# Optimization experiments

Hardware: AMD Instinct MI355X
Metric: run time of the kernel (lower is better)

Reference implementation:

```python
import jax, jax.numpy as jnp
import numpy as np

B, D, H, N, M, S = 64, 256, 512, 16384, 64, 3
EPS = 1e-4


def setup_inputs() -> dict:
    key = jax.random.key(0)
    ks = jax.random.split(key, 20)
    rn = lambda k, shape, sc=1.0: jax.random.normal(k, shape, dtype=jnp.float32) * sc
    z = lambda n: jnp.zeros((n,), jnp.float32)
    sc = 0.05
    return {
        "inp": rn(ks[0], (B, D)),
        "h_tm1": rn(ks[1], (B, H), 0.1),
        "c_tm1": rn(ks[2], (B, H), 0.1),
        "read_tm1": jax.nn.softmax(rn(ks[3], (B, N)), axis=-1),
        "write_tm1": jax.nn.softmax(rn(ks[4], (B, N)), axis=-1),
        "memory": rn(ks[5], (B, N, M), 0.1),
        "W_ih": rn(ks[6], (4 * H, D + M), sc), "b_ih": z(4 * H),
        "W_hh": rn(ks[7], (4 * H, H), sc), "b_hh": z(4 * H),
        "W_rk": rn(ks[8], (M, H), sc), "b_rk": z(M),
        "W_wk": rn(ks[9], (M, H), sc), "b_wk": z(M),
        "W_rc": rn(ks[10], (3, H), sc), "b_rc": z(3),
        "W_wc": rn(ks[11], (3, H), sc), "b_wc": z(3),
        "W_rs": rn(ks[12], (S, H), sc), "b_rs": z(S),
        "W_ws": rn(ks[13], (S, H), sc), "b_ws": z(S),
        "W_w": rn(ks[14], (2 * M, H), sc), "b_w": z(2 * M),
    }


def _head_params(h, Wk, bk, Wc, bc, Ws, bs):
    k = jnp.tanh(h @ Wk.T + bk)                 # [B, M] key
    c = h @ Wc.T + bc                           # [B, 3] beta/g/gamma raw
    s = jax.nn.softmax(h @ Ws.T + bs, axis=-1)  # [B, S] shift dist
    beta = jax.nn.relu(c[:, 0:1]) + EPS
    g = jax.nn.sigmoid(c[:, 1:2])
    gamma = jax.nn.relu(c[:, 2:3]) + 1.0 + EPS
    return k, s, beta, g, gamma


def _address(memory, w_tm1, k, s, beta, g, gamma):
    # content addressing: beta-scaled cosine similarity, softmax over slots
    dot = jnp.einsum('bm,bnm->bn', k, memory)                    # [B, N]
    nM = jnp.sqrt(jnp.sum(memory * memory, axis=-1)) + EPS       # [B, N]
    nk = jnp.sqrt(jnp.sum(k * k, axis=-1, keepdims=True)) + EPS  # [B, 1]
    content = jax.nn.softmax(beta * dot / (nM * nk), axis=-1)
    # interpolation with previous head
    inter = g * content + (1.0 - g) * w_tm1                      # [B, N]
    # circular shift conv: out[j] = sum_r s[r] * inter[(j + r - (S-1)) mod N]
    shifted = jnp.stack([jnp.roll(inter, S - 1 - r, axis=1) for r in range(S)], axis=-1)  # [B, N, S]
    conv = jnp.einsum('bns,bs->bn', shifted, s)
    # sharpening
    sharp = jnp.maximum(conv, 1e-8) ** gamma
    return sharp / jnp.sum(sharp, axis=1, keepdims=True)


def reference(inp, h_tm1, c_tm1, read_tm1, write_tm1, memory,
              W_ih, b_ih, W_hh, b_hh, W_rk, b_rk, W_wk, b_wk,
              W_rc, b_rc, W_wc, b_wc, W_rs, b_rs, W_ws, b_ws, W_w, b_w):
    # read head addressed from previous hidden state
    rk, rs, rbeta, rg, rgamma = _head_params(h_tm1, W_rk, b_rk, W_rc, b_rc, W_rs, b_rs)
    read_head = _address(memory, read_tm1, rk, rs, rbeta, rg, rgamma)
    M_read = jnp.einsum('bn,bnm->bm', read_head, memory)         # [B, M]
    # LSTMCell controller (torch gate order i, f, g, o)
    x = jnp.concatenate([inp, M_read], axis=1)
    gates = x @ W_ih.T + b_ih + h_tm1 @ W_hh.T + b_hh
    i, f, gg, o = jnp.split(gates, 4, axis=1)
    c_t = jax.nn.sigmoid(f) * c_tm1 + jax.nn.sigmoid(i) * jnp.tanh(gg)
    h_t = jax.nn.sigmoid(o) * jnp.tanh(c_t)
    # write head addressed from new hidden state
    wk, ws, wbeta, wg, wgamma = _head_params(h_t, W_wk, b_wk, W_wc, b_wc, W_ws, b_ws)
    write_head = _address(memory, write_tm1, wk, ws, wbeta, wg, wgamma)
    wa = h_t @ W_w.T + b_w
    e = jax.nn.sigmoid(wa[:, :M])                                # erase [B, M]
    a = wa[:, M:]                                                # add   [B, M]
    ww = write_head[:, :, None]                                  # [B, N, 1]
    M_out = memory * (1.0 - ww * e[:, None, :]) + ww * a[:, None, :]
    return (h_t, c_t, read_head, write_head, M_out)
```

## Files before the change

### kernel.cpp

```cpp
#include <hip/hip_runtime.h>
#include <hip/hip_bf16.h>
#include <math.h>

#define B_  64
#define D_  256
#define H_  512
#define N_  16384
#define M_  64
#define S_  3
#define EPS_ 1e-4f

__device__ __forceinline__ float sigmoidf_(float x) { return 1.0f / (1.0f + expf(-x)); }

template <bool WITH_W>
__global__ __launch_bounds__(256) void head_params_kernel(
    const float* __restrict__ h,
    const float* __restrict__ Wk, const float* __restrict__ bk,
    const float* __restrict__ Wc, const float* __restrict__ bc,
    const float* __restrict__ Ws, const float* __restrict__ bs,
    const float* __restrict__ Ww, const float* __restrict__ bw,
    float* __restrict__ k_out, float* __restrict__ nk_out,
    float* __restrict__ s_out,
    float* __restrict__ beta_out, float* __restrict__ g_out, float* __restrict__ gamma_out,
    float* __restrict__ e_out, float* __restrict__ a_out)
{
    const int b = blockIdx.x;
    const int tid = threadIdx.x;
    const int lane = tid & 63;
    const int wid = tid >> 6;
    __shared__ float raw[198];

    float h8[8];
    #pragma unroll
    for (int j = 0; j < 8; ++j) h8[j] = h[b * H_ + lane + 64 * j];

    const int count = WITH_W ? 198 : 70;
    for (int r = wid; r < count; r += 4) {
        const float* wrow;
        float bias;
        if (r < 64)       { wrow = Wk + r * H_;        bias = bk[r]; }
        else if (r < 67)  { wrow = Wc + (r - 64) * H_; bias = bc[r - 64]; }
        else if (r < 70)  { wrow = Ws + (r - 67) * H_; bias = bs[r - 67]; }
        else              { wrow = Ww + (r - 70) * H_; bias = bw[r - 70]; }
        float acc = 0.f;
        #pragma unroll
        for (int j = 0; j < 8; ++j) acc += wrow[lane + 64 * j] * h8[j];
        for (int off = 32; off >= 1; off >>= 1) acc += __shfl_xor(acc, off);
        if (lane == 0) raw[r] = acc + bias;
    }
    __syncthreads();

    if (tid < 64) {
        float kv = tanhf(raw[tid]);
        k_out[b * 64 + tid] = kv;
        float sq = kv * kv;
        for (int off = 32; off >= 1; off >>= 1) sq += __shfl_xor(sq, off);
        if (tid == 0) nk_out[b] = sqrtf(sq) + EPS_;
    } else if (tid == 64) {
        float c0 = raw[64], c1 = raw[65], c2 = raw[66];
        beta_out[b]  = fmaxf(c0, 0.f) + EPS_;
        g_out[b]     = sigmoidf_(c1);
        gamma_out[b] = fmaxf(c2, 0.f) + 1.f + EPS_;
    } else if (tid == 65) {
        float s0 = raw[67], s1 = raw[68], s2 = raw[69];
        float mx = fmaxf(s0, fmaxf(s1, s2));
        float e0 = expf(s0 - mx), e1 = expf(s1 - mx), e2 = expf(s2 - mx);
        float inv = 1.f / (e0 + e1 + e2);
        s_out[b * 3 + 0] = e0 * inv;
        s_out[b * 3 + 1] = e1 * inv;
        s_out[b * 3 + 2] = e2 * inv;
    }
    if (WITH_W && tid >= 128 && tid < 192) {
        int m = tid - 128;
        e_out[b * 64 + m] = sigmoidf_(raw[70 + m]);
        a_out[b * 64 + m] = raw[134 + m];
    }
}

template <bool COMPUTE_NM>
__global__ __launch_bounds__(256) void dot_kernel(
    const float* __restrict__ memory,
    const float* __restrict__ k,
    float* __restrict__ dot,
    float* __restrict__ nM)
{
    const int tid = threadIdx.x;
    const int lane = tid & 63;
    const int wid = tid >> 6;
    const int grp = lane >> 4;
    const int m16 = lane & 15;
    const int b = blockIdx.x >> 8;
    const int nbase = (blockIdx.x & 255) * 64;
    const float4 k4 = ((const float4*)(k + b * 64))[m16];
    const int slot = wid * 4 + grp;
    const size_t bbase = (size_t)b * N_;
    #pragma unroll
    for (int it = 0; it < 4; ++it) {
        const int n = nbase + it * 16 + slot;
        const float4 m4 = ((const float4*)(memory + (bbase + n) * 64))[m16];
        float d  = m4.x * k4.x + m4.y * k4.y + m4.z * k4.z + m4.w * k4.w;
        float sq = m4.x * m4.x + m4.y * m4.y + m4.z * m4.z + m4.w * m4.w;
        for (int off = 8; off >= 1; off >>= 1) {
            d += __shfl_xor(d, off);
            if (COMPUTE_NM) sq += __shfl_xor(sq, off);
        }
        if (m16 == 0) {
            dot[bbase + n] = d;
            if (COMPUTE_NM) nM[bbase + n] = sqrtf(sq) + EPS_;
        }
    }
}

__global__ __launch_bounds__(1024) void address_kernel(
    const float* __restrict__ dot,
    const float* __restrict__ nM,
    const float* __restrict__ w_tm1,
    const float* __restrict__ nk_a,
    const float* __restrict__ beta_a, const float* __restrict__ g_a,
    const float* __restrict__ gamma_a, const float* __restrict__ s_a,
    float* __restrict__ head_out)
{
    __shared__ float lds[N_];
    const int tid = threadIdx.x;
    const int b = blockIdx.x;
    const size_t base = (size_t)b * N_;
    const float beta = beta_a[b], g = g_a[b], gamma = gamma_a[b], nk = nk_a[b];
    const float s0 = s_a[b * 3 + 0], s1 = s_a[b * 3 + 1], s2 = s_a[b * 3 + 2];

    float lg[16];
    float lmax = -1e30f;
    #pragma unroll
    for (int t = 0; t < 16; ++t) {
        const int n = t * 1024 + tid;
        const float x = beta * dot[base + n] / (nM[base + n] * nk);
        lg[t] = x;
        lmax = fmaxf(lmax, x);
    }
    for (int off = 32; off >= 1; off >>= 1) lmax = fmaxf(lmax, __shfl_xor(lmax, off));
    if ((tid & 63) == 0) lds[tid >> 6] = lmax;
    __syncthreads();
    if (tid == 0) {
        float v = lds[0];
        for (int i = 1; i < 16; ++i) v = fmaxf(v, lds[i]);
        lds[16] = v;
    }
    __syncthreads();
    const float gmax = lds[16];

    float lsum = 0.f;
    #pragma unroll
    for (int t = 0; t < 16; ++t) { lg[t] = expf(lg[t] - gmax); lsum += lg[t]; }
    for (int off = 32; off >= 1; off >>= 1) lsum += __shfl_xor(lsum, off);
    if ((tid & 63) == 0) lds[tid >> 6] = lsum;
    __syncthreads();
    if (tid == 0) {
        float v = 0.f;
        for (int i = 0; i < 16; ++i) v += lds[i];
        lds[16] = v;
    }
    __syncthreads();
    const float inv_sum = 1.f / lds[16];
    __syncthreads();

    #pragma unroll
    for (int t = 0; t < 16; ++t) {
        const int n = t * 1024 + tid;
        lds[n] = g * lg[t] * inv_sum + (1.f - g) * w_tm1[base + n];
    }
    __syncthreads();

    float sh[16];
    float lsum2 = 0.f;
    #pragma unroll
    for (int t = 0; t < 16; ++t) {
        const int n = t * 1024 + tid;
        const float conv = s2 * lds[n] + s1 * lds[(n + N_ - 1) & (N_ - 1)]
                         + s0 * lds[(n + N_ - 2) & (N_ - 1)];
        const float v = powf(fmaxf(conv, 1e-8f), gamma);
        sh[t] = v;
        lsum2 += v;
    }
    __syncthreads();
    for (int off = 32; off >= 1; off >>= 1) lsum2 += __shfl_xor(lsum2, off);
    if ((tid & 63) == 0) lds[tid >> 6] = lsum2;
    __syncthreads();
    if (tid == 0) {
        float v = 0.f;
        for (int i = 0; i < 16; ++i) v += lds[i];
        lds[16] = v;
    }
    __syncthreads();
    const float inv2 = 1.f / lds[16];
    #pragma unroll
    for (int t = 0; t < 16; ++t) head_out[base + t * 1024 + tid] = sh[t] * inv2;
}

__global__ __launch_bounds__(256) void m_read_kernel(
    const float* __restrict__ memory,
    const float* __restrict__ head,
    float* __restrict__ M_read)
{
    const int tid = threadIdx.x;
    const int lane = tid & 63;
    const int wid = tid >> 6;
    const int grp = lane >> 4;
    const int m16 = lane & 15;
    const int b = blockIdx.x >> 6;
    const int nbase = (blockIdx.x & 63) * 256;
    const int slot = wid * 4 + grp;
    const size_t bbase = (size_t)b * N_;
    float4 acc = make_float4(0.f, 0.f, 0.f, 0.f);
    #pragma unroll 4
    for (int it = 0; it < 16; ++it) {
        const int n = nbase + it * 16 + slot;
        const float w = head[bbase + n];
        const float4 m4 = ((const float4*)(memory + (bbase + n) * 64))[m16];
        acc.x += w * m4.x; acc.y += w * m4.y; acc.z += w * m4.z; acc.w += w * m4.w;
    }
    for (int off = 32; off >= 16; off >>= 1) {
        acc.x += __shfl_xor(acc.x, off);
        acc.y += __shfl_xor(acc.y, off);
        acc.z += __shfl_xor(acc.z, off);
        acc.w += __shfl_xor(acc.w, off);
    }
    __shared__ float4 part[64];
    if (lane < 16) part[wid * 16 + lane] = acc;
    __syncthreads();
    if (tid < 16) {
        float4 t = part[tid];
        for (int w = 1; w < 4; ++w) {
            const float4 p = part[w * 16 + tid];
            t.x += p.x; t.y += p.y; t.z += p.z; t.w += p.w;
        }
        atomicAdd(&M_read[b * 64 + tid * 4 + 0], t.x);
        atomicAdd(&M_read[b * 64 + tid * 4 + 1], t.y);
        atomicAdd(&M_read[b * 64 + tid * 4 + 2], t.z);
        atomicAdd(&M_read[b * 64 + tid * 4 + 3], t.w);
    }
}

__global__ __launch_bounds__(256) void gates_splitk_kernel(
    const float* __restrict__ inp,
    const float* __restrict__ M_read,
    const float* __restrict__ h_tm1,
    const float* __restrict__ W_ih,
    const float* __restrict__ W_hh,
    float* __restrict__ gates)
{
    __shared__ __align__(16) float Xsm[64][68];
    __shared__ __align__(16) float Wsm[64][68];
    const int tid = threadIdx.x;
    const int jb = blockIdx.x & 31;
    const int c  = blockIdx.x >> 5;
    const int j0 = jb * 64;

    #pragma unroll
    for (int i = 0; i < 4; ++i) {
        const int e = i * 256 + tid;
        const int row = e >> 4;
        const int c4 = e & 15;
        const float* xrow;
        if (c < 4)       xrow = inp    + row * 256 + c * 64;
        else if (c == 4) xrow = M_read + row * 64;
        else             xrow = h_tm1  + row * 512 + (c - 5) * 64;
        const float4 v = ((const float4*)xrow)[c4];
        const int kl = c4 * 4;
        Xsm[kl + 0][row] = v.x; Xsm[kl + 1][row] = v.y;
        Xsm[kl + 2][row] = v.z; Xsm[kl + 3][row] = v.w;
    }
    #pragma unroll
    for (int i = 0; i < 4; ++i) {
        const int e = i * 256 + tid;
        const int row = e >> 4;
        const int c4 = e & 15;
        const float* wrow;
        if (c < 5) wrow = W_ih + (j0 + row) * 320 + c * 64;
        else       wrow = W_hh + (j0 + row) * 512 + (c - 5) * 64;
        const float4 v = ((const float4*)wrow)[c4];
        const int kl = c4 * 4;
        Wsm[kl + 0][row] = v.x; Wsm[kl + 1][row] = v.y;
        Wsm[kl + 2][row] = v.z; Wsm[kl + 3][row] = v.w;
    }
    __syncthreads();

    const int tx = tid & 15, ty = tid >> 4;
    float acc[4][4] = {};
    #pragma unroll
    for (int k = 0; k < 64; ++k) {
        const float4 av = *((const float4*)&Xsm[k][ty * 4]);
        const float4 wv = *((const float4*)&Wsm[k][tx * 4]);
        acc[0][0] += av.x * wv.x; acc[0][1] += av.x * wv.y; acc[0][2] += av.x * wv.z; acc[0][3] += av.x * wv.w;
        acc[1][0] += av.y * wv.x; acc[1][1] += av.y * wv.y; acc[1][2] += av.y * wv.z; acc[1][3] += av.y * wv.w;
        acc[2][0] += av.z * wv.x; acc[2][1] += av.z * wv.y; acc[2][2] += av.z * wv.z; acc[2][3] += av.z * wv.w;
        acc[3][0] += av.w * wv.x; acc[3][1] += av.w * wv.y; acc[3][2] += av.w * wv.z; acc[3][3] += av.w * wv.w;
    }
    #pragma unroll
    for (int bi = 0; bi < 4; ++bi) {
        const int b = ty * 4 + bi;
        #pragma unroll
        for (int ji = 0; ji < 4; ++ji) {
            atomicAdd(&gates[b * 2048 + j0 + tx * 4 + ji], acc[bi][ji]);
        }
    }
}

__global__ __launch_bounds__(256) void lstm_kernel(
    const float* __restrict__ gates,
    const float* __restrict__ b_ih, const float* __restrict__ b_hh,
    const float* __restrict__ c_tm1,
    float* __restrict__ h_out, float* __restrict__ c_out)
{
    const int idx = blockIdx.x * 256 + threadIdx.x;
    const int b = idx >> 9, j = idx & 511;
    const float* gr = gates + b * 2048;
    const float i_ = sigmoidf_(gr[j]        + b_ih[j]        + b_hh[j]);
    const float f_ = sigmoidf_(gr[512 + j]  + b_ih[512 + j]  + b_hh[512 + j]);
    const float g_ = tanhf(   gr[1024 + j] + b_ih[1024 + j] + b_hh[1024 + j]);
    const float o_ = sigmoidf_(gr[1536 + j] + b_ih[1536 + j] + b_hh[1536 + j]);
    const float c = f_ * c_tm1[idx] + i_ * g_;
    c_out[idx] = c;
    h_out[idx] = o_ * tanhf(c);
}

__global__ __launch_bounds__(256) void m_out_kernel(
    const float* __restrict__ memory,
    const float* __restrict__ whead,
    const float* __restrict__ e,
    const float* __restrict__ a,
    float* __restrict__ M_out)
{
    const size_t total = (size_t)B_ * N_ * 16;
    const size_t stride = (size_t)gridDim.x * 256;
    for (size_t idx = (size_t)blockIdx.x * 256 + threadIdx.x; idx < total; idx += stride) {
        const size_t nlin = idx >> 4;
        const int m4 = (int)(idx & 15);
        const int b = (int)(nlin >> 14);
        const float w = whead[nlin];
        const float4 ev = ((const float4*)(e + b * 64))[m4];
        const float4 av = ((const float4*)(a + b * 64))[m4];
        const float4 mv = ((const float4*)memory)[idx];
        float4 o;
        o.x = mv.x * (1.f - w * ev.x) + w * av.x;
        o.y = mv.y * (1.f - w * ev.y) + w * av.y;
        o.z = mv.z * (1.f - w * ev.z) + w * av.z;
        o.w = mv.w * (1.f - w * ev.w) + w * av.w;
        ((float4*)M_out)[idx] = o;
    }
}

extern "C" void kernel_launch(void* const* d_in, const int* in_sizes, int n_in,
                              void* d_out, int out_size, void* d_ws, size_t ws_size,
                              hipStream_t stream)
{
    const float* inp       = (const float*)d_in[0];
    const float* h_tm1     = (const float*)d_in[1];
    const float* c_tm1     = (const float*)d_in[2];
    const float* read_tm1  = (const float*)d_in[3];
    const float* write_tm1 = (const float*)d_in[4];
    const float* memory    = (const float*)d_in[5];
    const float* W_ih = (const float*)d_in[6];  const float* b_ih = (const float*)d_in[7];
    const float* W_hh = (const float*)d_in[8];  const float* b_hh = (const float*)d_in[9];
    const float* W_rk = (const float*)d_in[10]; const float* b_rk = (const float*)d_in[11];
    const float* W_wk = (const float*)d_in[12]; const float* b_wk = (const float*)d_in[13];
    const float* W_rc = (const float*)d_in[14]; const float* b_rc = (const float*)d_in[15];
    const float* W_wc = (const float*)d_in[16]; const float* b_wc = (const float*)d_in[17];
    const float* W_rs = (const float*)d_in[18]; const float* b_rs = (const float*)d_in[19];
    const float* W_ws = (const float*)d_in[20]; const float* b_ws = (const float*)d_in[21];
    const float* W_w  = (const float*)d_in[22]; const float* b_w  = (const float*)d_in[23];

    float* out = (float*)d_out;
    float* h_out   = out;
    float* c_out   = out + 32768;
    float* rhead   = out + 65536;
    float* whead   = out + 65536 + 1048576;
    float* Mout    = out + 65536 + 2 * 1048576;

    float* dot_r = rhead;
    float* dot_w = whead;
    float* nM    = Mout;

    float* ws = (float*)d_ws;
    float* gates  = ws;
    float* rk     = ws + 131072;
    float* wk     = ws + 135168;
    float* M_read = ws + 139264;
    float* e_buf  = ws + 143360;
    float* a_buf  = ws + 147456;
    float* rs     = ws + 151552;
    float* wss    = ws + 151744;
    float* rbeta  = ws + 151936;
    float* rg     = ws + 152000;
    float* rgamma = ws + 152064;
    float* rnk    = ws + 152128;
    float* wbeta  = ws + 152192;
    float* wg     = ws + 152256;
    float* wgamma = ws + 152320;
    float* wnk    = ws + 152384;

    hipMemsetAsync(M_read, 0, B_ * M_ * sizeof(float), stream);
    hipMemsetAsync(gates, 0, B_ * 4 * H_ * sizeof(float), stream);

    head_params_kernel<false><<<B_, 256, 0, stream>>>(
        h_tm1, W_rk, b_rk, W_rc, b_rc, W_rs, b_rs, nullptr, nullptr,
        rk, rnk, rs, rbeta, rg, rgamma, nullptr, nullptr);
    dot_kernel<true><<<B_ * 256, 256, 0, stream>>>(memory, rk, dot_r, nM);
    address_kernel<<<B_, 1024, 0, stream>>>(dot_r, nM, read_tm1, rnk, rbeta, rg, rgamma, rs, rhead);
    m_read_kernel<<<B_ * 64, 256, 0, stream>>>(memory, rhead, M_read);
    gates_splitk_kernel<<<13 * 32, 256, 0, stream>>>(inp, M_read, h_tm1, W_ih, W_hh, gates);
    lstm_kernel<<<128, 256, 0, stream>>>(gates, b_ih, b_hh, c_tm1, h_out, c_out);
    head_params_kernel<true><<<B_, 256, 0, stream>>>(
        h_out, W_wk, b_wk, W_wc, b_wc, W_ws, b_ws, W_w, b_w,
        wk, wnk, wss, wbeta, wg, wgamma, e_buf, a_buf);
    dot_kernel<false><<<B_ * 256, 256, 0, stream>>>(memory, wk, dot_w, nullptr);
    address_kernel<<<B_, 1024, 0, stream>>>(dot_w, nM, write_tm1, wnk, wbeta, wg, wgamma, wss, whead);
    m_out_kernel<<<16384, 256, 0, stream>>>(memory, whead, e_buf, a_buf, Mout);
}
```

Measured before the change: 781.7 us.

## Split addressing into wide-grid stages and fold normalization into consumers

The single 64-block address kernel is replaced by a score kernel that writes scaled cosine logits directly, a per-batch softmax statistics kernel, and a 4096-block interpolate/shift/sharpen kernel that atomically accumulates sums. The final sharpen normalization is folded into the M_read and M_out kernels, which also write the head outputs. This aims to raise parallelism over the low-occupancy 64-block kernel and drop a full pass over the head arrays, at the cost of extra launches, atomics and recomputing exp for neighbouring slots.

Result: slower. 817.7 us (+4.6%).

```diff
diff --git a/kernel.cpp b/kernel.cpp
--- a/kernel.cpp
+++ b/kernel.cpp
@@ -1,5 +1,4 @@
 #include <hip/hip_runtime.h>
-#include <hip/hip_bf16.h>
 #include <math.h>
 
 #define B_  64
@@ -77,12 +76,14 @@
     }
 }
 
-template <bool COMPUTE_NM>
-__global__ __launch_bounds__(256) void dot_kernel(
+template <int MODE>
+__global__ __launch_bounds__(256) void score_kernel(
     const float* __restrict__ memory,
     const float* __restrict__ k,
-    float* __restrict__ dot,
-    float* __restrict__ nM)
+    const float* __restrict__ beta_a,
+    const float* __restrict__ nk_a,
+    float* __restrict__ xout,
+    float* __restrict__ nMbuf)
 {
     const int tid = threadIdx.x;
     const int lane = tid & 63;
@@ -92,6 +93,7 @@
     const int b = blockIdx.x >> 8;
     const int nbase = (blockIdx.x & 255) * 64;
     const float4 k4 = ((const float4*)(k + b * 64))[m16];
+    const float beta = beta_a[b], nk = nk_a[b];
     const int slot = wid * 4 + grp;
     const size_t bbase = (size_t)b * N_;
     #pragma unroll
@@ -99,105 +101,106 @@
         const int n = nbase + it * 16 + slot;
         const float4 m4 = ((const float4*)(memory + (bbase + n) * 64))[m16];
         float d  = m4.x * k4.x + m4.y * k4.y + m4.z * k4.z + m4.w * k4.w;
-        float sq = m4.x * m4.x + m4.y * m4.y + m4.z * m4.z + m4.w * m4.w;
+        float sq = 0.f;
+        if (MODE == 0) sq = m4.x * m4.x + m4.y * m4.y + m4.z * m4.z + m4.w * m4.w;
         for (int off = 8; off >= 1; off >>= 1) {
             d += __shfl_xor(d, off);
-            if (COMPUTE_NM) sq += __shfl_xor(sq, off);
+            if (MODE == 0) sq += __shfl_xor(sq, off);
         }
         if (m16 == 0) {
-            dot[bbase + n] = d;
-            if (COMPUTE_NM) nM[bbase + n] = sqrtf(sq) + EPS_;
+            float nMv;
+            if (MODE == 0) {
+                nMv = sqrtf(sq) + EPS_;
+                nMbuf[bbase + n] = nMv;
+            } else {
+                nMv = nMbuf[bbase + n];
+            }
+            xout[bbase + n] = beta * d / (nMv * nk);
         }
     }
 }
 
-__global__ __launch_bounds__(1024) void address_kernel(
-    const float* __restrict__ dot,
-    const float* __restrict__ nM,
-    const float* __restrict__ w_tm1,
-    const float* __restrict__ nk_a,
-    const float* __restrict__ beta_a, const float* __restrict__ g_a,
-    const float* __restrict__ gamma_a, const float* __restrict__ s_a,
-    float* __restrict__ head_out)
-{
-    __shared__ float lds[N_];
+__global__ __launch_bounds__(1024) void softmax_stats_kernel(
+    const float* __restrict__ x,
+    float* __restrict__ gmax_a, float* __restrict__ ginv_a)
+{
+    __shared__ float red[17];
     const int tid = threadIdx.x;
     const int b = blockIdx.x;
     const size_t base = (size_t)b * N_;
-    const float beta = beta_a[b], g = g_a[b], gamma = gamma_a[b], nk = nk_a[b];
-    const float s0 = s_a[b * 3 + 0], s1 = s_a[b * 3 + 1], s2 = s_a[b * 3 + 2];
-
-    float lg[16];
+    const int wid = tid >> 6;
+
+    float lx[16];
     float lmax = -1e30f;
     #pragma unroll
     for (int t = 0; t < 16; ++t) {
-        const int n = t * 1024 + tid;
-        const float x = beta * dot[base + n] / (nM[base + n] * nk);
-        lg[t] = x;
-        lmax = fmaxf(lmax, x);
+        lx[t] = x[base + t * 1024 + tid];
+        lmax = fmaxf(lmax, lx[t]);
     }
     for (int off = 32; off >= 1; off >>= 1) lmax = fmaxf(lmax, __shfl_xor(lmax, off));
-    if ((tid & 63) == 0) lds[tid >> 6] = lmax;
+    if ((tid & 63) == 0) red[wid] = lmax;
     __syncthreads();
     if (tid == 0) {
-        float v = lds[0];
-        for (int i = 1; i < 16; ++i) v = fmaxf(v, lds[i]);
-        lds[16] = v;
-    }
-    __syncthreads();
-    const float gmax = lds[16];
+        float v = red[0];
+        for (int i = 1; i < 16; ++i) v = fmaxf(v, red[i]);
+        red[16] = v;
+    }
+    __syncthreads();
+    const float gmax = red[16];
+    __syncthreads();
 
     float lsum = 0.f;
     #pragma unroll
-    for (int t = 0; t < 16; ++t) { lg[t] = expf(lg[t] - gmax); lsum += lg[t]; }
+    for (int t = 0; t < 16; ++t) lsum += expf(lx[t] - gmax);
     for (int off = 32; off >= 1; off >>= 1) lsum += __shfl_xor(lsum, off);
-    if ((tid & 63) == 0) lds[tid >> 6] = lsum;
+    if ((tid & 63) == 0) red[wid] = lsum;
     __syncthreads();
     if (tid == 0) {
         float v = 0.f;
-        for (int i = 0; i < 16; ++i) v += lds[i];
-        lds[16] = v;
-    }
-    __syncthreads();
-    const float inv_sum = 1.f / lds[16];
-    __syncthreads();
-
-    #pragma unroll
-    for (int t = 0; t < 16; ++t) {
-        const int n = t * 1024 + tid;
-        lds[n] = g * lg[t] * inv_sum + (1.f - g) * w_tm1[base + n];
-    }
-    __syncthreads();
-
-    float sh[16];
-    float lsum2 = 0.f;
-    #pragma unroll
-    for (int t = 0; t < 16; ++t) {
-        const int n = t * 1024 + tid;
-        const float conv = s2 * lds[n] + s1 * lds[(n + N_ - 1) & (N_ - 1)]
-                         + s0 * lds[(n + N_ - 2) & (N_ - 1)];
-        const float v = powf(fmaxf(conv, 1e-8f), gamma);
-        sh[t] = v;
-        lsum2 += v;
-    }
-    __syncthreads();
-    for (int off = 32; off >= 1; off >>= 1) lsum2 += __shfl_xor(lsum2, off);
-    if ((tid & 63) == 0) lds[tid >> 6] = lsum2;
-    __syncthreads();
-    if (tid == 0) {
-        float v = 0.f;
-        for (int i = 0; i < 16; ++i) v += lds[i];
-        lds[16] = v;
-    }
-    __syncthreads();
-    const float inv2 = 1.f / lds[16];
-    #pragma unroll
-    for (int t = 0; t < 16; ++t) head_out[base + t * 1024 + tid] = sh[t] * inv2;
-}
-
-__global__ __launch_bounds__(256) void m_read_kernel(
+        for (int i = 0; i < 16; ++i) v += red[i];
+        gmax_a[b] = gmax;
+        ginv_a[b] = 1.f / v;
+    }
+}
+
+__global__ __launch_bounds__(256) void conv_sharp_kernel(
+    const float* __restrict__ x,
+    const float* __restrict__ w_tm1,
+    const float* __restrict__ gmax_a, const float* __restrict__ ginv_a,
+    const float* __restrict__ g_a, const float* __restrict__ gamma_a,
+    const float* __restrict__ s_a,
+    float* __restrict__ sharp, float* __restrict__ ssum)
+{
+    __shared__ float red[4];
+    const int tid = threadIdx.x;
+    const int b = blockIdx.x >> 6;
+    const int n = (blockIdx.x & 63) * 256 + tid;
+    const size_t base = (size_t)b * N_;
+    const float gmax = gmax_a[b], ginv = ginv_a[b];
+    const float g = g_a[b], gamma = gamma_a[b];
+    const float s0 = s_a[b * 3 + 0], s1 = s_a[b * 3 + 1], s2 = s_a[b * 3 + 2];
+
+    const int n1 = (n + N_ - 1) & (N_ - 1);
+    const int n2 = (n + N_ - 2) & (N_ - 1);
+    const float i0 = g * expf(x[base + n]  - gmax) * ginv + (1.f - g) * w_tm1[base + n];
+    const float i1 = g * expf(x[base + n1] - gmax) * ginv + (1.f - g) * w_tm1[base + n1];
+    const float i2 = g * expf(x[base + n2] - gmax) * ginv + (1.f - g) * w_tm1[base + n2];
+    const float conv = s2 * i0 + s1 * i1 + s0 * i2;
+    const float v = powf(fmaxf(conv, 1e-8f), gamma);
+    sharp[base + n] = v;
+
+    float lsum = v;
+    for (int off = 32; off >= 1; off >>= 1) lsum += __shfl_xor(lsum, off);
+    if ((tid & 63) == 0) red[tid >> 6] = lsum;
+    __syncthreads();
+    if (tid == 0) atomicAdd(&ssum[b], red[0] + red[1] + red[2] + red[3]);
+}
+
+__global__ __launch_bounds__(256) void mread_norm_kernel(
     const float* __restrict__ memory,
-    const float* __restrict__ head,
+    const float* __restrict__ sharp,
+    const float* __restrict__ ssum,
+    float* __restrict__ rhead,
     float* __restrict__ M_read)
 {
     const int tid = threadIdx.x;
@@ -209,12 +212,14 @@
     const int nbase = (blockIdx.x & 63) * 256;
     const int slot = wid * 4 + grp;
     const size_t bbase = (size_t)b * N_;
+    const float inv2 = 1.f / ssum[b];
     float4 acc = make_float4(0.f, 0.f, 0.f, 0.f);
     #pragma unroll 4
     for (int it = 0; it < 16; ++it) {
         const int n = nbase + it * 16 + slot;
-        const float w = head[bbase + n];
+        const float w = sharp[bbase + n] * inv2;
         const float4 m4 = ((const float4*)(memory + (bbase + n) * 64))[m16];
+        if (m16 == 0) rhead[bbase + n] = w;
         acc.x += w * m4.x; acc.y += w * m4.y; acc.z += w * m4.z; acc.w += w * m4.w;
     }
     for (int off = 32; off >= 16; off >>= 1) {
@@ -322,11 +327,13 @@
     h_out[idx] = o_ * tanhf(c);
 }
 
-__global__ __launch_bounds__(256) void m_out_kernel(
+__global__ __launch_bounds__(256) void mout_norm_kernel(
     const float* __restrict__ memory,
-    const float* __restrict__ whead,
+    const float* __restrict__ sharpw,
+    const float* __restrict__ ssum_w,
     const float* __restrict__ e,
     const float* __restrict__ a,
+    float* __restrict__ whead,
     float* __restrict__ M_out)
 {
     const size_t total = (size_t)B_ * N_ * 16;
@@ -335,10 +342,11 @@
         const size_t nlin = idx >> 4;
         const int m4 = (int)(idx & 15);
         const int b = (int)(nlin >> 14);
-        const float w = whead[nlin];
+        const float w = sharpw[nlin] * (1.f / ssum_w[b]);
         const float4 ev = ((const float4*)(e + b * 64))[m4];
         const float4 av = ((const float4*)(a + b * 64))[m4];
         const float4 mv = ((const float4*)memory)[idx];
+        if (m4 == 0) whead[nlin] = w;
         float4 o;
         o.x = mv.x * (1.f - w * ev.x) + w * av.x;
         o.y = mv.y * (1.f - w * ev.y) + w * av.y;
@@ -369,49 +377,63 @@
     const float* W_w  = (const float*)d_in[22]; const float* b_w  = (const float*)d_in[23];
 
     float* out = (float*)d_out;
-    float* h_out   = out;
-    float* c_out   = out + 32768;
-    float* rhead   = out + 65536;
-    float* whead   = out + 65536 + 1048576;
-    float* Mout    = out + 65536 + 2 * 1048576;
-
-    float* dot_r = rhead;
-    float* dot_w = whead;
-    float* nM    = Mout;
+    float* h_out = out;
+    float* c_out = out + 32768;
+    float* rhead = out + 65536;
+    float* whead = out + 65536 + 1048576;
+    float* Mout  = out + 65536 + 2 * 1048576;
+
+    float* x_r     = rhead;
+    float* sharp_r = whead;
+    float* x_w     = Mout;
+    float* nMbuf   = Mout + (size_t)B_ * N_;
+    float* sharp_w = whead;
 
     float* ws = (float*)d_ws;
     float* gates  = ws;
-    float* rk     = ws + 131072;
-    float* wk     = ws + 135168;
-    float* M_read = ws + 139264;
-    float* e_buf  = ws + 143360;
-    float* a_buf  = ws + 147456;
-    float* rs     = ws + 151552;
-    float* wss    = ws + 151744;
-    float* rbeta  = ws + 151936;
-    float* rg     = ws + 152000;
-    float* rgamma = ws + 152064;
-    float* rnk    = ws + 152128;
-    float* wbeta  = ws + 152192;
-    float* wg     = ws + 152256;
-    float* wgamma = ws + 152320;
-    float* wnk    = ws + 152384;
-
-    hipMemsetAsync(M_read, 0, B_ * M_ * sizeof(float), stream);
-    hipMemsetAsync(gates, 0, B_ * 4 * H_ * sizeof(float), stream);
+    float* M_read = ws + 131072;
+    float* ssum_r = ws + 135168;
+    float* ssum_w = ws + 135232;
+    float* rk     = ws + 135296;
+    float* wk     = ws + 139392;
+    float* e_buf  = ws + 143488;
+    float* a_buf  = ws + 147584;
+    float* rs     = ws + 151680;
+    float* wss    = ws + 151872;
+    float* rbeta  = ws + 152064;
+    float* rg     = ws + 152128;
+    float* rgamma = ws + 152192;
+    float* rnk    = ws + 152256;
+    float* wbeta  = ws + 152320;
+    float* wg     = ws + 152384;
+    float* wgamma = ws + 152448;
+    float* wnk    = ws + 152512;
+    float* gmax_r = ws + 152576;
+    float* ginv_r = ws + 152640;
+    float* gmax_w = ws + 152704;
+    float* ginv_w = ws + 152768;
+
+    hipMemsetAsync(gates, 0, (131072 + 4096 + 64 + 64) * sizeof(float), stream);
 
     head_params_kernel<false><<<B_, 256, 0, stream>>>(
         h_tm1, W_rk, b_rk, W_rc, b_rc, W_rs, b_rs, nullptr, nullptr,
         rk, rnk, rs, rbeta, rg, rgamma, nullptr, nullptr);
-    dot_kernel<true><<<B_ * 256, 256, 0, stream>>>(memory, rk, dot_r, nM);
-    address_kernel<<<B_, 1024, 0, stream>>>(dot_r, nM, read_tm1, rnk, rbeta, rg, rgamma, rs, rhead);
-    m_read_kernel<<<B_ * 64, 256, 0, stream>>>(memory, rhead, M_read);
+    score_kernel<0><<<B_ * 256, 256, 0, stream>>>(memory, rk, rbeta, rnk, x_r, nMbuf);
+    softmax_stats_kernel<<<B_, 1024, 0, stream>>>(x_r, gmax_r, ginv_r);
+    conv_sharp_kernel<<<B_ * 64, 256, 0, stream>>>(
+        x_r, read_tm1, gmax_r, ginv_r, rg, rgamma, rs, sharp_r, ssum_r);
+    mread_norm_kernel<<<B_ * 64, 256, 0, stream>>>(memory, sharp_r, ssum_r, rhead, M_read);
+
     gates_splitk_kernel<<<13 * 32, 256, 0, stream>>>(inp, M_read, h_tm1, W_ih, W_hh, gates);
     lstm_kernel<<<128, 256, 0, stream>>>(gates, b_ih, b_hh, c_tm1, h_out, c_out);
+
     head_params_kernel<true><<<B_, 256, 0, stream>>>(
         h_out, W_wk, b_wk, W_wc, b_wc, W_ws, b_ws, W_w, b_w,
         wk, wnk, wss, wbeta, wg, wgamma, e_buf, a_buf);
-    dot_kernel<false><<<B_ * 256, 256, 0, stream>>>(memory, wk, dot_w, nullptr);
-    address_kernel<<<B_, 1024, 0, stream>>>(dot_w, nM, write_tm1, wnk, wbeta, wg, wgamma, wss, whead);
-    m_out_kernel<<<16384, 256, 0, stream>>>(memory, whead, e_buf, a_buf, Mout);
-}
+    score_kernel<1><<<B_ * 256, 256, 0, stream>>>(memory, wk, wbeta, wnk, x_w, nMbuf);
+    softmax_stats_kernel<<<B_, 1024, 0, stream>>>(x_w, gmax_w, ginv_w);
+    conv_sharp_kernel<<<B_ * 64, 256, 0, stream>>>(
+        x_w, write_tm1, gmax_w, ginv_w, wg, wgamma, wss, sharp_w, ssum_w);
+    mout_norm_kernel<<<16384, 256, 0, stream>>>(
+        memory, sharp_w, ssum_w, e_buf, a_buf, whead, Mout);
+}
```
